# Kernel tuning notes

Hardware: AMD Instinct MI355X
Metric: run time of the kernel (lower is better)

## Reference

```python
import jax, jax.numpy as jnp
import numpy as np

T = 500            # diffusion steps (conf.T)
NS = 516           # struc_vocab_size = 4 special + 512 VQVAE codes
NQ = 33            # seq_vocab_size
MASK_S = 3         # C.STRUCTURE_MASK_TOKEN
MASK_Q = 32        # C.SEQUENCE_MASK_TOKEN
B, L = 256, 1024
EPS = 1e-10


def _alpha_schedule():
    # beta = 1 / (T - t + 1), alpha = cumprod(1 - beta) ; shape (T+1,)
    beta = 1.0 / (T - jnp.arange(T + 1, dtype=jnp.float32) + 1.0)
    return jnp.cumprod(1.0 - beta, axis=-1)


def setup_inputs() -> dict:
    key = jax.random.key(0)
    k1, k2, k3 = jax.random.split(key, 3)
    structure = jax.random.randint(k1, (B, L), 0, NS)
    sequence = jax.random.randint(k2, (B, L), 0, NQ)
    t = jax.random.randint(k3, (B,), 1, T + 1)   # t in [1, T]
    return {"structure": structure, "sequence": sequence, "t": t,
            "alpha": _alpha_schedule()}


def _q_sample(key, x0, t, alpha, N, mask_idx):
    # Row x0 of the absorbing q_mat is: alpha[t]*e_{x0} + (1-alpha[t])*e_{mask}.
    # This is exactly probs = _at(x0, absorbing_q_mat(...)) without the
    # O(N^2) matrix build.
    a = alpha[t][:, None, None]                      # (B,1,1)
    probs = a * jax.nn.one_hot(x0, N, dtype=alpha.dtype)  # (B,L,N)
    probs = probs.at[..., mask_idx].add((1.0 - a)[..., 0])
    # multinomial(num_samples=1) == categorical sample from probs
    return jax.random.categorical(key, jnp.log(probs + EPS), axis=-1)


def reference(structure, sequence, t, alpha):
    key = jax.random.key(42)
    ks, kq = jax.random.split(key)
    noised_structure = _q_sample(ks, structure, t, alpha, NS, MASK_S)
    noised_sequence = _q_sample(kq, sequence, t, alpha, NQ, MASK_Q)
    return (noised_structure, noised_sequence, t)
```

## Files before the change

kernel.cpp:

```cpp
#include <hip/hip_runtime.h>
#include <math.h>
#include <stdint.h>


#define B_CONST 256
#define L_CONST 1024
#define NS_CONST 516
#define NQ_CONST 33
#define MASK_S 3
#define MASK_Q 32
#define ROWS (B_CONST * L_CONST)

__host__ __device__ inline void tf_round(uint32_t& x0, uint32_t& x1, int r) {
  x0 += x1;
  x1 = (x1 << r) | (x1 >> (32 - r));
  x1 ^= x0;
}

__host__ __device__ inline void threefry2x32(uint32_t k0, uint32_t k1,
                                             uint32_t x0, uint32_t x1,
                                             uint32_t& o0, uint32_t& o1) {
  const uint32_t ks2 = k0 ^ k1 ^ 0x1BD11BDAu;
  x0 += k0; x1 += k1;
  tf_round(x0, x1, 13); tf_round(x0, x1, 15); tf_round(x0, x1, 26); tf_round(x0, x1, 6);
  x0 += k1; x1 += ks2 + 1u;
  tf_round(x0, x1, 17); tf_round(x0, x1, 29); tf_round(x0, x1, 16); tf_round(x0, x1, 24);
  x0 += ks2; x1 += k0 + 2u;
  tf_round(x0, x1, 13); tf_round(x0, x1, 15); tf_round(x0, x1, 26); tf_round(x0, x1, 6);
  x0 += k0; x1 += k1 + 3u;
  tf_round(x0, x1, 17); tf_round(x0, x1, 29); tf_round(x0, x1, 16); tf_round(x0, x1, 24);
  x0 += k1; x1 += ks2 + 4u;
  tf_round(x0, x1, 13); tf_round(x0, x1, 15); tf_round(x0, x1, 26); tf_round(x0, x1, 6);
  x0 += ks2; x1 += k0 + 5u;
  o0 = x0; o1 = x1;
}

__device__ inline float gumbel_from_bits(uint32_t bits) {
  const float tiny = 1.1754943508222875e-38f;
  float f = __uint_as_float((bits >> 9) | 0x3f800000u) - 1.0f;
  float u = fmaxf(tiny, f + tiny);
  float nl = -(float)log((double)u);
  return -(float)log((double)nl);
}

__device__ inline float log_cr(float x) { return (float)log((double)x); }

__device__ inline int sample_row(uint32_t k0, uint32_t k1, uint32_t row,
                                 int N, int M, int x, float a) {
  if (x == M) return M;
  const float EPSf = 1e-10f;
  const float lx = log_cr(a + EPSf);
  const float lm = log_cr((1.0f - a) + EPSf);
  const uint32_t base = row * (uint32_t)N;
  uint32_t ox0, ox1, om0, om1;
  threefry2x32(k0, k1, 0u, base + (uint32_t)x, ox0, ox1);
  threefry2x32(k0, k1, 0u, base + (uint32_t)M, om0, om1);
  const float vx = gumbel_from_bits(ox0 ^ ox1) + lx;
  const float vm = gumbel_from_bits(om0 ^ om1) + lm;
  if (x < M) return (vx >= vm) ? x : M;
  return (vm >= vx) ? M : x;
}

__global__ __launch_bounds__(256)
void d3pm_kernel(const int* __restrict__ structure,
                 const int* __restrict__ sequence,
                 const int* __restrict__ tv,
                 const float* __restrict__ alpha,
                 int* __restrict__ out,
                 uint32_t ks0, uint32_t ks1, uint32_t kq0, uint32_t kq1) {
  const int gid = blockIdx.x * 256 + threadIdx.x;
  if (gid < ROWS) {
    const int b = gid >> 10;
    const float a = alpha[tv[b]];
    out[gid] = sample_row(ks0, ks1, (uint32_t)gid, NS_CONST, MASK_S,
                          structure[gid], a);
  } else if (gid < 2 * ROWS) {
    const int r = gid - ROWS;
    const int b = r >> 10;
    const float a = alpha[tv[b]];
    out[gid] = sample_row(kq0, kq1, (uint32_t)r, NQ_CONST, MASK_Q,
                          sequence[r], a);
  } else if (gid < 2 * ROWS + B_CONST) {
    out[gid] = tv[gid - 2 * ROWS];
  }
}

extern "C" void kernel_launch(void* const* d_in, const int* in_sizes, int n_in,
                              void* d_out, int out_size, void* d_ws, size_t ws_size,
                              hipStream_t stream) {
  (void)in_sizes; (void)n_in; (void)out_size; (void)d_ws; (void)ws_size;
  const int*   structure = (const int*)d_in[0];
  const int*   sequence  = (const int*)d_in[1];
  const int*   t         = (const int*)d_in[2];
  const float* alpha     = (const float*)d_in[3];
  int* out = (int*)d_out;

  uint32_t ks0, ks1, kq0, kq1;
  threefry2x32(0u, 42u, 0u, 0u, ks0, ks1);
  threefry2x32(0u, 42u, 0u, 1u, kq0, kq1);

  const int total = 2 * ROWS + B_CONST;
  d3pm_kernel<<<(total + 255) / 256, 256, 0, stream>>>(
      structure, sequence, t, alpha, out, ks0, ks1, kq0, kq1);
}
```

Measured before the change: 69.90 us.

## Vectorize to four rows per thread and use fast Gumbel with exact fallback

```diff
diff --git a/kernel.cpp b/kernel.cpp
--- a/kernel.cpp
+++ b/kernel.cpp
@@ -10,6 +10,9 @@
 #define MASK_S 3
 #define MASK_Q 32
 #define ROWS (B_CONST * L_CONST)
+#define QUADS (ROWS / 4)
+#define QUADS_T (B_CONST / 4)
+#define TOTAL_THREADS (2 * QUADS + QUADS_T)
 
 __host__ __device__ inline void tf_round(uint32_t& x0, uint32_t& x1, int r) {
   x0 += x1;
@@ -35,7 +38,7 @@
   o0 = x0; o1 = x1;
 }
 
-__device__ inline float gumbel_from_bits(uint32_t bits) {
+__device__ inline float gumbel_exact(uint32_t bits) {
   const float tiny = 1.1754943508222875e-38f;
   float f = __uint_as_float((bits >> 9) | 0x3f800000u) - 1.0f;
   float u = fmaxf(tiny, f + tiny);
@@ -43,45 +46,76 @@
   return -(float)log((double)nl);
 }
 
+__device__ inline float gumbel_fast(uint32_t bits) {
+  const float tiny = 1.1754943508222875e-38f;
+  float f = __uint_as_float((bits >> 9) | 0x3f800000u) - 1.0f;
+  float u = fmaxf(tiny, f + tiny);
+  float nl = (u >= 0.5f) ? -log1pf(u - 1.0f) : -__logf(u);
+  return -__logf(nl);
+}
+
 __device__ inline float log_cr(float x) { return (float)log((double)x); }
 
-__device__ inline int sample_row(uint32_t k0, uint32_t k1, uint32_t row,
-                                 int N, int M, int x, float a) {
+template <int N, int M>
+__device__ inline int decide(uint32_t k0, uint32_t k1, uint32_t row,
+                             int x, float lx, float lm) {
   if (x == M) return M;
-  const float EPSf = 1e-10f;
-  const float lx = log_cr(a + EPSf);
-  const float lm = log_cr((1.0f - a) + EPSf);
   const uint32_t base = row * (uint32_t)N;
   uint32_t ox0, ox1, om0, om1;
   threefry2x32(k0, k1, 0u, base + (uint32_t)x, ox0, ox1);
   threefry2x32(k0, k1, 0u, base + (uint32_t)M, om0, om1);
-  const float vx = gumbel_from_bits(ox0 ^ ox1) + lx;
-  const float vm = gumbel_from_bits(om0 ^ om1) + lm;
-  if (x < M) return (vx >= vm) ? x : M;
-  return (vm >= vx) ? M : x;
+  const uint32_t bx = ox0 ^ ox1, bm = om0 ^ om1;
+  float d = (gumbel_fast(bx) + lx) - (gumbel_fast(bm) + lm);
+  if (fabsf(d) <= 2.5e-4f) {
+    float vx = gumbel_exact(bx) + lx;
+    float vm = gumbel_exact(bm) + lm;
+    if (x < M) return (vx >= vm) ? x : M;
+    return (vm >= vx) ? M : x;
+  }
+  return (d > 0.0f) ? x : M;
 }
 
 __global__ __launch_bounds__(256)
-void d3pm_kernel(const int* __restrict__ structure,
-                 const int* __restrict__ sequence,
+void d3pm_kernel(const int4* __restrict__ structure4,
+                 const int4* __restrict__ sequence4,
                  const int* __restrict__ tv,
                  const float* __restrict__ alpha,
-                 int* __restrict__ out,
+                 int4* __restrict__ out4,
                  uint32_t ks0, uint32_t ks1, uint32_t kq0, uint32_t kq1) {
-  const int gid = blockIdx.x * 256 + threadIdx.x;
-  if (gid < ROWS) {
-    const int b = gid >> 10;
+  const int tid = blockIdx.x * 256 + threadIdx.x;
+  const float EPSf = 1e-10f;
+
+  if (tid < QUADS) {
+    const int q = tid;
+    const int b = q >> 8;
     const float a = alpha[tv[b]];
-    out[gid] = sample_row(ks0, ks1, (uint32_t)gid, NS_CONST, MASK_S,
-                          structure[gid], a);
-  } else if (gid < 2 * ROWS) {
-    const int r = gid - ROWS;
-    const int b = r >> 10;
+    const float lx = log_cr(a + EPSf);
+    const float lm = log_cr((1.0f - a) + EPSf);
+    const uint32_t r0 = (uint32_t)(4 * q);
+    int4 xs = structure4[q];
+    int4 o;
+    o.x = decide<NS_CONST, MASK_S>(ks0, ks1, r0 + 0u, xs.x, lx, lm);
+    o.y = decide<NS_CONST, MASK_S>(ks0, ks1, r0 + 1u, xs.y, lx, lm);
+    o.z = decide<NS_CONST, MASK_S>(ks0, ks1, r0 + 2u, xs.z, lx, lm);
+    o.w = decide<NS_CONST, MASK_S>(ks0, ks1, r0 + 3u, xs.w, lx, lm);
+    out4[q] = o;
+  } else if (tid < 2 * QUADS) {
+    const int q = tid - QUADS;
+    const int b = q >> 8;
     const float a = alpha[tv[b]];
-    out[gid] = sample_row(kq0, kq1, (uint32_t)r, NQ_CONST, MASK_Q,
-                          sequence[r], a);
-  } else if (gid < 2 * ROWS + B_CONST) {
-    out[gid] = tv[gid - 2 * ROWS];
+    const float lx = log_cr(a + EPSf);
+    const float lm = log_cr((1.0f - a) + EPSf);
+    const uint32_t r0 = (uint32_t)(4 * q);
+    int4 xs = sequence4[q];
+    int4 o;
+    o.x = decide<NQ_CONST, MASK_Q>(kq0, kq1, r0 + 0u, xs.x, lx, lm);
+    o.y = decide<NQ_CONST, MASK_Q>(kq0, kq1, r0 + 1u, xs.y, lx, lm);
+    o.z = decide<NQ_CONST, MASK_Q>(kq0, kq1, r0 + 2u, xs.z, lx, lm);
+    o.w = decide<NQ_CONST, MASK_Q>(kq0, kq1, r0 + 3u, xs.w, lx, lm);
+    out4[QUADS + q] = o;
+  } else if (tid < TOTAL_THREADS) {
+    const int q = tid - 2 * QUADS;
+    out4[2 * QUADS + q] = ((const int4*)tv)[q];
   }
 }
 
@@ -93,13 +127,12 @@
   const int*   sequence  = (const int*)d_in[1];
   const int*   t         = (const int*)d_in[2];
   const float* alpha     = (const float*)d_in[3];
-  int* out = (int*)d_out;
 
   uint32_t ks0, ks1, kq0, kq1;
   threefry2x32(0u, 42u, 0u, 0u, ks0, ks1);
   threefry2x32(0u, 42u, 0u, 1u, kq0, kq1);
 
-  const int total = 2 * ROWS + B_CONST;
-  d3pm_kernel<<<(total + 255) / 256, 256, 0, stream>>>(
-      structure, sequence, t, alpha, out, ks0, ks1, kq0, kq1);
+  d3pm_kernel<<<(TOTAL_THREADS + 255) / 256, 256, 0, stream>>>(
+      (const int4*)structure, (const int4*)sequence, t, alpha,
+      (int4*)d_out, ks0, ks1, kq0, kq1);
 }
```

Measured after the change: 67.94 us. -2.8%, faster.
